# Kernel tuning notes

Hardware: AMD Instinct MI355X
Metric: run time of the kernel (lower is better)

Reference implementation:

```python
import jax, jax.numpy as jnp
import numpy as np

N, E, IN, ED, H, C, G, NC = 50000, 800000, 128, 32, 4, 16, 64, 2
HC = H * C  # 64
NEG_SLOPE = 0.2
EPS = 1e-5


def _layernorm(x, g, b):
    mu = jnp.mean(x, axis=-1, keepdims=True)
    var = jnp.mean((x - mu) ** 2, axis=-1, keepdims=True)
    return (x - mu) * jax.lax.rsqrt(var + EPS) * g + b


def _gat(x, src, dst, edge_attr, W, a_src, a_dst, We, a_edge, b):
    """PyG GATConv (v1) with edge features, concat=True."""
    n = x.shape[0]
    h, c = a_src.shape
    xw = (x @ W).reshape(n, h, c)                       # [N,H,C]
    al_src = jnp.sum(xw * a_src, axis=-1)               # [N,H]
    al_dst = jnp.sum(xw * a_dst, axis=-1)               # [N,H]
    ew = (edge_attr @ We).reshape(-1, h, c)             # [Ef,H,C]
    al_e = jnp.sum(ew * a_edge, axis=-1)                # [Ef,H]
    alpha = al_src[src] + al_dst[dst] + al_e            # [Ef,H]
    alpha = jnp.where(alpha > 0, alpha, NEG_SLOPE * alpha)
    # segment softmax over incoming edges of each dst node
    amax = jax.ops.segment_max(alpha, dst, num_segments=n)
    amax = jnp.where(jnp.isfinite(amax), amax, 0.0)
    ex = jnp.exp(alpha - amax[dst])
    denom = jax.ops.segment_sum(ex, dst, num_segments=n)
    att = ex / (denom[dst] + 1e-16)                     # [Ef,H]
    msg = xw[src] * att[:, :, None]                     # [Ef,H,C]
    out = jax.ops.segment_sum(msg, dst, num_segments=n) # [N,H,C]
    return out.reshape(n, h * c) + b


def setup_inputs() -> dict:
    ks = jax.random.split(jax.random.key(0), 24)
    s = 0.1
    inp = {
        "x": jax.random.normal(ks[0], (N, IN), jnp.float32),
        "edge_attr": jax.random.normal(ks[1], (E, ED), jnp.float32),
        "W1": jax.random.normal(ks[2], (IN, HC), jnp.float32) * s,
        "as1": jax.random.normal(ks[3], (H, C), jnp.float32) * s,
        "ad1": jax.random.normal(ks[4], (H, C), jnp.float32) * s,
        "We1": jax.random.normal(ks[5], (ED, HC), jnp.float32) * s,
        "ae1": jax.random.normal(ks[6], (H, C), jnp.float32) * s,
        "b1": jnp.zeros((HC,), jnp.float32),
        "W2": jax.random.normal(ks[7], (HC, HC), jnp.float32) * s,
        "as2": jax.random.normal(ks[8], (H, C), jnp.float32) * s,
        "ad2": jax.random.normal(ks[9], (H, C), jnp.float32) * s,
        "We2": jax.random.normal(ks[10], (ED, HC), jnp.float32) * s,
        "ae2": jax.random.normal(ks[11], (H, C), jnp.float32) * s,
        "b2": jnp.zeros((HC,), jnp.float32),
        "g1": jnp.ones((HC,), jnp.float32),
        "be1": jnp.zeros((HC,), jnp.float32),
        "fw1": jax.random.normal(ks[12], (HC, 32), jnp.float32) * s,
        "fb1": jnp.zeros((32,), jnp.float32),
        "g2": jnp.ones((32,), jnp.float32),
        "be2": jnp.zeros((32,), jnp.float32),
        "fw2": jax.random.normal(ks[13], (32, NC), jnp.float32) * s,
        "fb2": jnp.zeros((NC,), jnp.float32),
        "edge_index": jax.random.randint(ks[14], (2, E), 0, N, jnp.int64),
        "batch": jnp.sort(jax.random.randint(ks[15], (N,), 0, G, jnp.int64)),
    }
    return inp


def reference(x, edge_attr, W1, as1, ad1, We1, ae1, b1, W2, as2, ad2, We2, ae2,
              b2, g1, be1, fw1, fb1, g2, be2, fw2, fb2, edge_index, batch):
    src, dst = edge_index[0], edge_index[1]
    e = edge_attr.shape[0]
    # add_self_loops with fill_value='mean' (mean of incoming edge_attr per node)
    cnt = jax.ops.segment_sum(jnp.ones((e,), x.dtype), dst, num_segments=N)
    loop_ea = jax.ops.segment_sum(edge_attr, dst, num_segments=N) / jnp.clip(cnt, 1.0)[:, None]
    ar = jnp.arange(N)
    src_f = jnp.concatenate([src, ar])
    dst_f = jnp.concatenate([dst, ar])
    ea_f = jnp.concatenate([edge_attr, loop_ea], axis=0)

    h = _gat(x, src_f, dst_f, ea_f, W1, as1, ad1, We1, ae1, b1)
    h = jax.nn.relu(h)
    h = _layernorm(h, g1, be1)
    h = _gat(h, src_f, dst_f, ea_f, W2, as2, ad2, We2, ae2, b2)
    h = jax.nn.relu(h)
    pooled = jax.ops.segment_max(h, batch, num_segments=G)   # global_max_pool
    pooled = jnp.where(jnp.isfinite(pooled), pooled, 0.0)
    z = pooled @ fw1 + fb1
    z = _layernorm(z, g2, be2)
    z = jax.nn.relu(z)
    # dropout(p=0.4) is identity in eval mode
    z = z @ fw2 + fb2
    return jax.nn.log_softmax(z, axis=1)
```

## Files before the change

kernel.cpp:

```cpp
#include <hip/hip_runtime.h>
#include <math.h>

#define N_NODES 50000
#define N_EDGES 800000
#define IN_DIM 128
#define ED_DIM 32
#define NH 4
#define CH 16
#define HC 64
#define NG 64
#define NCL 2
#define NEG_SLOPE 0.2f
#define LN_EPS 1e-5f
#define NBLK1 196
#define NB_TILE 3125
#define NB_ECH 3125

__global__ void k_scan_local(const int* __restrict__ cnt, int* __restrict__ tmp_ex,
                             int* __restrict__ bsum) {
    __shared__ int sd[256];
    int t = threadIdx.x, idx = blockIdx.x * 256 + t;
    int v = (idx < N_NODES) ? cnt[idx] : 0;
    sd[t] = v; __syncthreads();
    for (int off = 1; off < 256; off <<= 1) {
        int add = (t >= off) ? sd[t - off] : 0;
        __syncthreads();
        sd[t] += add;
        __syncthreads();
    }
    if (idx < N_NODES) tmp_ex[idx] = sd[t] - v;
    if (t == 255) bsum[blockIdx.x] = sd[t];
}

__global__ __launch_bounds__(256) void k_phase1(
        const float* __restrict__ X, const float* __restrict__ W,
        const float* __restrict__ AS, const float* __restrict__ AD,
        float* __restrict__ XW, float* __restrict__ ALS, float* __restrict__ ALD,
        const float* __restrict__ ea,
        const float* __restrict__ We1, const float* __restrict__ ae1,
        const float* __restrict__ We2, const float* __restrict__ ae2,
        float4* __restrict__ ale8,
        const int* __restrict__ dst, int* __restrict__ cnt, int* __restrict__ rank_e) {
    __shared__ float smem[IN_DIM * HC + 16 * IN_DIM];
    int job = blockIdx.x % 3;
    int bid = blockIdx.x / 3;
    int t = threadIdx.x;
    if (job == 0) {
        const int K = IN_DIM;
        float* sW = smem;
        float* sX = smem + K * HC;
        for (int i = t; i < K * HC; i += 256) sW[i] = W[i];
        int nb = bid * 16;
        for (int i = t; i < 16 * K; i += 256) sX[i] = X[(long long)nb * K + i];
        __syncthreads();
        int sub = t >> 6, j = t & 63;
        float acc[4] = {0.f, 0.f, 0.f, 0.f};
        #pragma unroll 8
        for (int k = 0; k < K; ++k) {
            float wv = sW[k * HC + j];
            #pragma unroll
            for (int q = 0; q < 4; ++q) acc[q] += sX[(sub + 4 * q) * K + k] * wv;
        }
        float as_ = AS[j], ad_ = AD[j];
        #pragma unroll
        for (int q = 0; q < 4; ++q) {
            int n = nb + sub + 4 * q;
            XW[(long long)n * HC + j] = acc[q];
            float vs = acc[q] * as_, vd = acc[q] * ad_;
            #pragma unroll
            for (int m = 1; m < 16; m <<= 1) { vs += __shfl_xor(vs, m); vd += __shfl_xor(vd, m); }
            if ((j & 15) == 0) {
                int h = j >> 4;
                ALS[n * 4 + h] = vs; ALD[n * 4 + h] = vd;
            }
        }
    } else if (job == 1) {
        float* sVe = smem;
        float* sE  = smem + 256;
        {
            int d = t >> 3, k = t & 7;
            int l = k >> 2, h = k & 3;
            const float* We = l ? We2 : We1;
            const float* ae = l ? ae2 : ae1;
            float s = 0.f;
            #pragma unroll
            for (int c = 0; c < CH; ++c) s += We[d * HC + h * CH + c] * ae[h * CH + c];
            sVe[d * 8 + k] = s;
        }
        {
            const float4* gsrc = (const float4*)ea + (size_t)bid * 2048;
            #pragma unroll
            for (int r = 0; r < 8; ++r) {
                int i4 = t + r * 256;
                float4 v = gsrc[i4];
                float* dp = sE + (i4 >> 3) * 33 + ((i4 & 7) << 2);
                dp[0] = v.x; dp[1] = v.y; dp[2] = v.z; dp[3] = v.w;
            }
        }
        __syncthreads();
        int e = bid * 256 + t;
        float a[8];
        #pragma unroll
        for (int k = 0; k < 8; ++k) a[k] = 0.f;
        const float* row = sE + t * 33;
        #pragma unroll
        for (int q = 0; q < ED_DIM / 4; ++q) {
            #pragma unroll
            for (int u = 0; u < 4; ++u) {
                float ev = row[q * 4 + u];
                #pragma unroll
                for (int k = 0; k < 8; ++k) a[k] += ev * sVe[(q * 4 + u) * 8 + k];
            }
        }
        float4* out = ale8 + (long long)e * 2;
        out[0] = make_float4(a[0], a[1], a[2], a[3]);
        out[1] = make_float4(a[4], a[5], a[6], a[7]);
    } else {
        int e = bid * 256 + t;
        if (e < N_EDGES) rank_e[e] = atomicAdd(&cnt[dst[e]], 1);
    }
}

__global__ void k_scan_perm(const int* __restrict__ tmp_ex, const int* __restrict__ bsum,
                            int* __restrict__ row_start,
                            const int* __restrict__ dst, const int* __restrict__ srcI,
                            const int* __restrict__ rank_e, int2* __restrict__ perm_src) {
    __shared__ int sd[256];
    __shared__ int sboff[256];
    int t = threadIdx.x;
    int v = (t < NBLK1) ? bsum[t] : 0;
    sd[t] = v; __syncthreads();
    for (int off = 1; off < 256; off <<= 1) {
        int add = (t >= off) ? sd[t - off] : 0;
        __syncthreads();
        sd[t] += add;
        __syncthreads();
    }
    sboff[t] = sd[t] - v;
    __syncthreads();
    if (blockIdx.x < NBLK1) {
        int idx = blockIdx.x * 256 + t;
        if (idx < N_NODES) row_start[idx] = tmp_ex[idx] + sboff[blockIdx.x];
        if (idx == 0) row_start[N_NODES] = N_EDGES;
    } else {
        int e = (blockIdx.x - NBLK1) * 256 + t;
        if (e < N_EDGES) {
            int d = dst[e];
            int pos = tmp_ex[d] + sboff[d >> 8] + rank_e[e];
            perm_src[pos] = make_int2(e, srcI[e]);
        }
    }
}

__global__ __launch_bounds__(256) void k_agg1x(
        const int* __restrict__ rs, const int2* __restrict__ ps,
        const float* __restrict__ ale8,
        const float* __restrict__ ALS, const float* __restrict__ ALD,
        const float* __restrict__ XW, const float* __restrict__ bias,
        const float* __restrict__ gam, const float* __restrict__ bet,
        const float* __restrict__ W2,
        const float* __restrict__ AS2, const float* __restrict__ AD2,
        float* __restrict__ XW2, float* __restrict__ ALS2, float* __restrict__ ALD2) {
    __shared__ float sW2[HC * HC];
    __shared__ float sh[4][HC];
    int t = threadIdx.x;
    for (int i = t; i < HC * HC; i += 256) sW2[i] = W2[i];
    __syncthreads();
    int wid = t >> 6;
    int n = blockIdx.x * 4 + wid;
    int lane = t & 63;
    int h = lane >> 4;
    int e0 = rs[n], e1 = rs[n + 1];
    float adn = ALD[n * 4 + h];
    float acc0 = 0.f, l0 = 0.f, as0 = 0.f;
    float acc1 = 0.f, l1 = 0.f, as1 = 0.f;
    float acc2 = 0.f, l2 = 0.f, as2 = 0.f;
    float acc3 = 0.f, l3 = 0.f, as3 = 0.f;
    int e = e0;
    for (; e + 3 < e1; e += 4) {
        int2 pA = ps[e], pB = ps[e + 1], pC = ps[e + 2], pD = ps[e + 3];
        float aeA = ale8[(long long)pA.x * 8 + h];
        float aeB = ale8[(long long)pB.x * 8 + h];
        float aeC = ale8[(long long)pC.x * 8 + h];
        float aeD = ale8[(long long)pD.x * 8 + h];
        float xA = XW[pA.y * HC + lane];
        float xB = XW[pB.y * HC + lane];
        float xC = XW[pC.y * HC + lane];
        float xD = XW[pD.y * HC + lane];
        float aA = ALS[pA.y * 4 + h] + adn + aeA;
        float aB = ALS[pB.y * 4 + h] + adn + aeB;
        float aC = ALS[pC.y * 4 + h] + adn + aeC;
        float aD = ALS[pD.y * 4 + h] + adn + aeD;
        aA = aA > 0.f ? aA : NEG_SLOPE * aA;
        aB = aB > 0.f ? aB : NEG_SLOPE * aB;
        aC = aC > 0.f ? aC : NEG_SLOPE * aC;
        aD = aD > 0.f ? aD : NEG_SLOPE * aD;
        float qA = __expf(aA), qB = __expf(aB), qC = __expf(aC), qD = __expf(aD);
        acc0 += qA * xA; l0 += qA; as0 += aeA;
        acc1 += qB * xB; l1 += qB; as1 += aeB;
        acc2 += qC * xC; l2 += qC; as2 += aeC;
        acc3 += qD * xD; l3 += qD; as3 += aeD;
    }
    for (; e < e1; ++e) {
        int2 pA = ps[e];
        float aeA = ale8[(long long)pA.x * 8 + h];
        float xA = XW[pA.y * HC + lane];
        float aA = ALS[pA.y * 4 + h] + adn + aeA;
        aA = aA > 0.f ? aA : NEG_SLOPE * aA;
        float qA = __expf(aA);
        acc0 += qA * xA; l0 += qA; as0 += aeA;
    }
    int d = e1 - e0;
    float invd = 1.f / (float)(d > 0 ? d : 1);
    float aSelf = ALS[n * 4 + h] + adn + (as0 + as1 + as2 + as3) * invd;
    aSelf = aSelf > 0.f ? aSelf : NEG_SLOPE * aSelf;
    float pS = __expf(aSelf);
    float acc = (acc0 + acc1) + (acc2 + acc3) + pS * XW[n * HC + lane];
    float l = (l0 + l1) + (l2 + l3) + pS;
    float v = acc / (l + 1e-16f) + bias[lane];
    v = fmaxf(v, 0.f);
    {
        float s1 = v;
        #pragma unroll
        for (int mm = 1; mm < 64; mm <<= 1) s1 += __shfl_xor(s1, mm);
        float mean = s1 * (1.f / 64.f);
        float dd = v - mean;
        float s2 = dd * dd;
        #pragma unroll
        for (int mm = 1; mm < 64; mm <<= 1) s2 += __shfl_xor(s2, mm);
        float var = s2 * (1.f / 64.f);
        v = dd * rsqrtf(var + LN_EPS) * gam[lane] + bet[lane];
    }
    sh[wid][lane] = v;
    float a2 = 0.f;
    #pragma unroll 8
    for (int k = 0; k < HC; ++k) a2 += sh[wid][k] * sW2[k * HC + lane];
    XW2[(long long)n * HC + lane] = a2;
    float vs = a2 * AS2[lane], vd = a2 * AD2[lane];
    #pragma unroll
    for (int m = 1; m < 16; m <<= 1) { vs += __shfl_xor(vs, m); vd += __shfl_xor(vd, m); }
    if ((lane & 15) == 0) {
        ALS2[n * 4 + h] = vs; ALD2[n * 4 + h] = vd;
    }
}

template<bool DO_LN, int LOFF>
__global__ void k_agg(const int* __restrict__ rs, const int2* __restrict__ ps,
                      const float* __restrict__ ale8,
                      const float* __restrict__ ALS, const float* __restrict__ ALD,
                      const float* __restrict__ XW, const float* __restrict__ bias,
                      const float* __restrict__ gam, const float* __restrict__ bet,
                      float* __restrict__ OUT) {
    int n = (blockIdx.x * blockDim.x + threadIdx.x) >> 6;
    if (n >= N_NODES) return;
    int lane = threadIdx.x & 63;
    int h = lane >> 4;
    int e0 = rs[n], e1 = rs[n + 1];
    float adn = ALD[n * 4 + h];
    float acc0 = 0.f, l0 = 0.f, as0 = 0.f;
    float acc1 = 0.f, l1 = 0.f, as1 = 0.f;
    float acc2 = 0.f, l2 = 0.f, as2 = 0.f;
    float acc3 = 0.f, l3 = 0.f, as3 = 0.f;
    int e = e0;
    for (; e + 3 < e1; e += 4) {
        int2 pA = ps[e], pB = ps[e + 1], pC = ps[e + 2], pD = ps[e + 3];
        float aeA = ale8[(long long)pA.x * 8 + LOFF + h];
        float aeB = ale8[(long long)pB.x * 8 + LOFF + h];
        float aeC = ale8[(long long)pC.x * 8 + LOFF + h];
        float aeD = ale8[(long long)pD.x * 8 + LOFF + h];
        float xA = XW[pA.y * HC + lane];
        float xB = XW[pB.y * HC + lane];
        float xC = XW[pC.y * HC + lane];
        float xD = XW[pD.y * HC + lane];
        float aA = ALS[pA.y * 4 + h] + adn + aeA;
        float aB = ALS[pB.y * 4 + h] + adn + aeB;
        float aC = ALS[pC.y * 4 + h] + adn + aeC;
        float aD = ALS[pD.y * 4 + h] + adn + aeD;
        aA = aA > 0.f ? aA : NEG_SLOPE * aA;
        aB = aB > 0.f ? aB : NEG_SLOPE * aB;
        aC = aC > 0.f ? aC : NEG_SLOPE * aC;
        aD = aD > 0.f ? aD : NEG_SLOPE * aD;
        float qA = __expf(aA), qB = __expf(aB), qC = __expf(aC), qD = __expf(aD);
        acc0 += qA * xA; l0 += qA; as0 += aeA;
        acc1 += qB * xB; l1 += qB; as1 += aeB;
        acc2 += qC * xC; l2 += qC; as2 += aeC;
        acc3 += qD * xD; l3 += qD; as3 += aeD;
    }
    for (; e < e1; ++e) {
        int2 pA = ps[e];
        float aeA = ale8[(long long)pA.x * 8 + LOFF + h];
        float xA = XW[pA.y * HC + lane];
        float aA = ALS[pA.y * 4 + h] + adn + aeA;
        aA = aA > 0.f ? aA : NEG_SLOPE * aA;
        float qA = __expf(aA);
        acc0 += qA * xA; l0 += qA; as0 += aeA;
    }
    int d = e1 - e0;
    float invd = 1.f / (float)(d > 0 ? d : 1);
    float aSelf = ALS[n * 4 + h] + adn + (as0 + as1 + as2 + as3) * invd;
    aSelf = aSelf > 0.f ? aSelf : NEG_SLOPE * aSelf;
    float pS = __expf(aSelf);
    float acc = (acc0 + acc1) + (acc2 + acc3) + pS * XW[n * HC + lane];
    float l = (l0 + l1) + (l2 + l3) + pS;
    float v = acc / (l + 1e-16f) + bias[lane];
    v = fmaxf(v, 0.f);
    if (DO_LN) {
        float s1 = v;
        #pragma unroll
        for (int mm = 1; mm < 64; mm <<= 1) s1 += __shfl_xor(s1, mm);
        float mean = s1 * (1.f / 64.f);
        float dd = v - mean;
        float s2 = dd * dd;
        #pragma unroll
        for (int mm = 1; mm < 64; mm <<= 1) s2 += __shfl_xor(s2, mm);
        float var = s2 * (1.f / 64.f);
        v = dd * rsqrtf(var + LN_EPS) * gam[lane] + bet[lane];
    }
    OUT[(long long)n * HC + lane] = v;
}

__global__ void k_pool(const float* __restrict__ H2, const int* __restrict__ batch,
                       float* __restrict__ pooled) {
    int j = threadIdx.x & 63;
    int r = threadIdx.x >> 6;
    int base = blockIdx.x * 128;
    int gcur = -1; float rm = 0.f;
    for (int n = base + r; n < base + 128 && n < N_NODES; n += 4) {
        int g = batch[n];
        if (g != gcur) {
            if (gcur >= 0) atomicMax((unsigned int*)&pooled[gcur * HC + j], __float_as_uint(rm));
            gcur = g; rm = 0.f;
        }
        rm = fmaxf(rm, H2[(long long)n * HC + j]);
    }
    if (gcur >= 0) atomicMax((unsigned int*)&pooled[gcur * HC + j], __float_as_uint(rm));
}

__global__ void k_head(const float* __restrict__ pooled,
                       const float* __restrict__ fw1, const float* __restrict__ fb1,
                       const float* __restrict__ g2, const float* __restrict__ be2,
                       const float* __restrict__ fw2, const float* __restrict__ fb2,
                       float* __restrict__ out) {
    int g = blockIdx.x;
    int j = threadIdx.x;
    float z = 0.f;
    if (j < 32) {
        for (int k = 0; k < HC; ++k) z += pooled[g * HC + k] * fw1[k * 32 + j];
        z += fb1[j];
    }
    float s1 = (j < 32) ? z : 0.f;
    for (int m = 1; m < 32; m <<= 1) s1 += __shfl_xor(s1, m, 32);
    float mean = s1 * (1.f / 32.f);
    float d = z - mean;
    float s2 = (j < 32) ? d * d : 0.f;
    for (int m = 1; m < 32; m <<= 1) s2 += __shfl_xor(s2, m, 32);
    float var = s2 * (1.f / 32.f);
    float zz = 0.f;
    if (j < 32) {
        zz = d * rsqrtf(var + LN_EPS) * g2[j] + be2[j];
        zz = fmaxf(zz, 0.f);
    }
    float p0 = (j < 32) ? zz * fw2[j * NCL + 0] : 0.f;
    float p1 = (j < 32) ? zz * fw2[j * NCL + 1] : 0.f;
    for (int m = 1; m < 32; m <<= 1) { p0 += __shfl_xor(p0, m, 32); p1 += __shfl_xor(p1, m, 32); }
    if (j == 0) {
        float l0 = p0 + fb2[0], l1 = p1 + fb2[1];
        float mx = fmaxf(l0, l1);
        float ls = mx + logf(__expf(l0 - mx) + __expf(l1 - mx));
        out[g * NCL + 0] = l0 - ls;
        out[g * NCL + 1] = l1 - ls;
    }
}

extern "C" void kernel_launch(void* const* d_in, const int* in_sizes, int n_in,
                              void* d_out, int out_size, void* d_ws, size_t ws_size,
                              hipStream_t stream) {
    const float* x   = (const float*)d_in[0];
    const float* ea  = (const float*)d_in[1];
    const float* W1  = (const float*)d_in[2];
    const float* as1 = (const float*)d_in[3];
    const float* ad1 = (const float*)d_in[4];
    const float* We1 = (const float*)d_in[5];
    const float* ae1 = (const float*)d_in[6];
    const float* b1  = (const float*)d_in[7];
    const float* W2  = (const float*)d_in[8];
    const float* as2 = (const float*)d_in[9];
    const float* ad2 = (const float*)d_in[10];
    const float* We2 = (const float*)d_in[11];
    const float* ae2 = (const float*)d_in[12];
    const float* b2  = (const float*)d_in[13];
    const float* g1  = (const float*)d_in[14];
    const float* be1 = (const float*)d_in[15];
    const float* fw1 = (const float*)d_in[16];
    const float* fb1 = (const float*)d_in[17];
    const float* g2  = (const float*)d_in[18];
    const float* be2 = (const float*)d_in[19];
    const float* fw2 = (const float*)d_in[20];
    const float* fb2 = (const float*)d_in[21];
    const int* eidx  = (const int*)d_in[22];
    const int* batch = (const int*)d_in[23];
    const int* srcI = eidx;
    const int* dstI = eidx + N_EDGES;

    char* w = (char*)d_ws;
    auto alloc = [&](size_t bytes) { char* p = w; w += (bytes + 255) & ~(size_t)255; return p; };
    int*   cnt       = (int*)  alloc((size_t)N_NODES * 4);
    int*   row_start = (int*)  alloc((size_t)(N_NODES + 1) * 4);
    int*   rank_e    = (int*)  alloc((size_t)N_EDGES * 4);
    int*   tmp_ex    = (int*)  alloc((size_t)N_NODES * 4);
    int*   bsum      = (int*)  alloc(256 * 4);
    int2*  perm_src  = (int2*) alloc((size_t)N_EDGES * 8);
    float4* ale8     = (float4*)alloc((size_t)N_EDGES * 32);
    float* xw1       = (float*)alloc((size_t)N_NODES * HC * 4);
    float* als1      = (float*)alloc((size_t)N_NODES * 4 * 4);
    float* ald1      = (float*)alloc((size_t)N_NODES * 4 * 4);
    float* xw2       = (float*)alloc((size_t)N_NODES * HC * 4);
    float* als2      = (float*)alloc((size_t)N_NODES * 4 * 4);
    float* ald2      = (float*)alloc((size_t)N_NODES * 4 * 4);
    float* h2        = (float*)alloc((size_t)N_NODES * HC * 4);
    float* pooled    = (float*)alloc((size_t)NG * HC * 4);

    hipMemsetAsync(cnt, 0, (size_t)N_NODES * 4, stream);
    hipMemsetAsync(pooled, 0, (size_t)NG * HC * 4, stream);

    k_phase1<<<3 * NB_TILE, 256, 0, stream>>>(x, W1, as1, ad1, xw1, als1, ald1,
                                              ea, We1, ae1, We2, ae2, ale8,
                                              dstI, cnt, rank_e);
    k_scan_local<<<NBLK1, 256, 0, stream>>>(cnt, tmp_ex, bsum);
    k_scan_perm<<<NBLK1 + NB_ECH, 256, 0, stream>>>(tmp_ex, bsum, row_start,
                                                    dstI, srcI, rank_e, perm_src);

    k_agg1x<<<N_NODES / 4, 256, 0, stream>>>(row_start, perm_src, (const float*)ale8,
                                             als1, ald1, xw1, b1, g1, be1,
                                             W2, as2, ad2, xw2, als2, ald2);
    k_agg<false, 4><<<N_NODES / 4, 256, 0, stream>>>(row_start, perm_src, (const float*)ale8,
                                                     als2, ald2, xw2, b2, nullptr, nullptr, h2);

    k_pool<<<(N_NODES + 127) / 128, 256, 0, stream>>>(h2, batch, pooled);
    k_head<<<NG, 64, 0, stream>>>(pooled, fw1, fb1, g2, be2, fw2, fb2, (float*)d_out);
}
```

Measured before the change: 409.6 us.

## Fuse whole GAT pipeline into one cooperative persistent kernel with grid syncs

```diff
diff --git a/kernel.cpp b/kernel.cpp
--- a/kernel.cpp
+++ b/kernel.cpp
@@ -1,12 +1,13 @@
 #include <hip/hip_runtime.h>
+#include <hip/hip_cooperative_groups.h>
 #include <math.h>
+
+namespace cg = cooperative_groups;
 
 #define N_NODES 50000
 #define N_EDGES 800000
 #define IN_DIM 128
 #define ED_DIM 32
-#define NH 4
-#define CH 16
 #define HC 64
 #define NG 64
 #define NCL 2
@@ -14,22 +15,354 @@
 #define LN_EPS 1e-5f
 #define NBLK1 196
 #define NB_TILE 3125
-#define NB_ECH 3125
-
-__global__ void k_scan_local(const int* __restrict__ cnt, int* __restrict__ tmp_ex,
-                             int* __restrict__ bsum) {
-    __shared__ int sd[256];
-    int t = threadIdx.x, idx = blockIdx.x * 256 + t;
-    int v = (idx < N_NODES) ? cnt[idx] : 0;
-    sd[t] = v; __syncthreads();
-    for (int off = 1; off < 256; off <<= 1) {
-        int add = (t >= off) ? sd[t - off] : 0;
+#define NVB_B 12500
+#define NVB_D 3321
+#define NVB_AGG 12500
+#define NVB_POOL 391
+#define NVB_HEAD 16
+
+struct MParams {
+    const float *x, *ea, *W1, *as1, *ad1, *We1, *ae1, *b1;
+    const float *W2, *as2, *ad2, *We2, *ae2, *b2, *g1, *be1;
+    const float *fw1, *fb1, *g2, *be2, *fw2, *fb2;
+    const int *srcI, *dstI, *batch;
+    int *cnt, *row_start, *rank_e, *tmp_ex, *bsum;
+    int2 *perm_src;
+    float4 *ale8;
+    float *xw1, *als1, *ald1, *xw2, *als2, *ald2, *h2, *pooled, *out;
+};
+
+__global__ __launch_bounds__(256, 8) void mega(MParams p) {
+    cg::grid_group grid = cg::this_grid();
+    __shared__ float smem[4608];
+    int t = threadIdx.x;
+    int nb = gridDim.x;
+
+    for (int i = blockIdx.x * 256 + t; i < N_NODES; i += nb * 256) p.cnt[i] = 0;
+    for (int i = blockIdx.x * 256 + t; i < NG * HC; i += nb * 256) p.pooled[i] = 0.f;
+    grid.sync();
+
+    for (int vb = blockIdx.x; vb < NVB_B; vb += nb) {
+        int job = vb & 3;
+        int bid = vb >> 2;
+        if (job == 0) {
+            float* sX = smem;
+            float* sW = smem + 2048;
+            int nbase = bid * 16;
+            for (int i = t; i < 16 * IN_DIM; i += 256)
+                sX[i] = p.x[(long long)nbase * IN_DIM + i];
+            int sub = t >> 6, j = t & 63;
+            float acc[4] = {0.f, 0.f, 0.f, 0.f};
+            for (int c = 0; c < IN_DIM; c += 32) {
+                if (c) __syncthreads();
+                for (int i = t; i < 32 * HC; i += 256) sW[i] = p.W1[c * HC + i];
+                __syncthreads();
+                #pragma unroll 8
+                for (int kk = 0; kk < 32; ++kk) {
+                    float wv = sW[kk * HC + j];
+                    #pragma unroll
+                    for (int q = 0; q < 4; ++q)
+                        acc[q] += sX[(sub + 4 * q) * IN_DIM + c + kk] * wv;
+                }
+            }
+            float as_ = p.as1[j], ad_ = p.ad1[j];
+            #pragma unroll
+            for (int q = 0; q < 4; ++q) {
+                int n = nbase + sub + 4 * q;
+                p.xw1[(long long)n * HC + j] = acc[q];
+                float vs = acc[q] * as_, vd = acc[q] * ad_;
+                #pragma unroll
+                for (int m = 1; m < 16; m <<= 1) { vs += __shfl_xor(vs, m); vd += __shfl_xor(vd, m); }
+                if ((j & 15) == 0) {
+                    int h = j >> 4;
+                    p.als1[n * 4 + h] = vs; p.ald1[n * 4 + h] = vd;
+                }
+            }
+        } else if (job == 2) {
+            int e = bid * 256 + t;
+            p.rank_e[e] = atomicAdd(&p.cnt[p.dstI[e]], 1);
+        } else {
+            int ebid = (bid << 1) | (job >> 1);
+            float* sVe = smem;
+            float* sE  = smem + 256;
+            {
+                int d = t >> 3, k = t & 7;
+                int l = k >> 2, h = k & 3;
+                const float* We = l ? p.We2 : p.We1;
+                const float* ae = l ? p.ae2 : p.ae1;
+                float s = 0.f;
+                #pragma unroll
+                for (int c = 0; c < 16; ++c) s += We[d * HC + h * 16 + c] * ae[h * 16 + c];
+                sVe[d * 8 + k] = s;
+            }
+            const float4* gsrc = (const float4*)p.ea + (size_t)ebid * 1024;
+            #pragma unroll
+            for (int r = 0; r < 4; ++r) {
+                int i4 = t + r * 256;
+                float4 v = gsrc[i4];
+                float* dp = sE + (i4 >> 3) * 33 + ((i4 & 7) << 2);
+                dp[0] = v.x; dp[1] = v.y; dp[2] = v.z; dp[3] = v.w;
+            }
+            __syncthreads();
+            int el = t & 127;
+            int kb = (t >> 7) * 4;
+            long long e = (long long)ebid * 128 + el;
+            const float* row = sE + el * 33;
+            float a0 = 0.f, a1 = 0.f, a2 = 0.f, a3 = 0.f;
+            #pragma unroll
+            for (int c = 0; c < ED_DIM; ++c) {
+                float ev = row[c];
+                a0 += ev * sVe[c * 8 + kb];
+                a1 += ev * sVe[c * 8 + kb + 1];
+                a2 += ev * sVe[c * 8 + kb + 2];
+                a3 += ev * sVe[c * 8 + kb + 3];
+            }
+            p.ale8[e * 2 + (t >> 7)] = make_float4(a0, a1, a2, a3);
+        }
         __syncthreads();
-        sd[t] += add;
+    }
+    grid.sync();
+
+    {
+        int* sd = (int*)smem;
+        for (int vb = blockIdx.x; vb < NBLK1; vb += nb) {
+            int idx = vb * 256 + t;
+            int v = (idx < N_NODES) ? p.cnt[idx] : 0;
+            sd[t] = v; __syncthreads();
+            for (int off = 1; off < 256; off <<= 1) {
+                int add = (t >= off) ? sd[t - off] : 0;
+                __syncthreads();
+                sd[t] += add;
+                __syncthreads();
+            }
+            if (idx < N_NODES) p.tmp_ex[idx] = sd[t] - v;
+            if (t == 255) p.bsum[vb] = sd[t];
+            __syncthreads();
+        }
+    }
+    grid.sync();
+
+    {
+        int* sd = (int*)smem;
+        int* sboff = sd + 256;
+        for (int vb = blockIdx.x; vb < NVB_D; vb += nb) {
+            int v = (t < NBLK1) ? p.bsum[t] : 0;
+            sd[t] = v; __syncthreads();
+            for (int off = 1; off < 256; off <<= 1) {
+                int add = (t >= off) ? sd[t - off] : 0;
+                __syncthreads();
+                sd[t] += add;
+                __syncthreads();
+            }
+            sboff[t] = sd[t] - v;
+            __syncthreads();
+            if (vb < NBLK1) {
+                int idx = vb * 256 + t;
+                if (idx < N_NODES) p.row_start[idx] = p.tmp_ex[idx] + sboff[vb];
+                if (idx == 0) p.row_start[N_NODES] = N_EDGES;
+            } else {
+                int e = (vb - NBLK1) * 256 + t;
+                int d = p.dstI[e];
+                int pos = p.tmp_ex[d] + sboff[d >> 8] + p.rank_e[e];
+                p.perm_src[pos] = make_int2(e, p.srcI[e]);
+            }
+            __syncthreads();
+        }
+    }
+    grid.sync();
+
+    {
+        float* sW2 = smem;
+        float* sh  = smem + 4096;
+        for (int i = t; i < HC * HC; i += 256) sW2[i] = p.W2[i];
         __syncthreads();
-    }
-    if (idx < N_NODES) tmp_ex[idx] = sd[t] - v;
-    if (t == 255) bsum[blockIdx.x] = sd[t];
+        int wid = t >> 6, lane = t & 63, h = lane >> 4;
+        for (int vb = blockIdx.x; vb < NVB_AGG; vb += nb) {
+            int n = vb * 4 + wid;
+            int e0 = p.row_start[n], e1 = p.row_start[n + 1];
+            float adn = p.ald1[n * 4 + h];
+            float acc0 = 0.f, l0 = 0.f, as0 = 0.f;
+            float acc1 = 0.f, l1 = 0.f, as1 = 0.f;
+            float acc2 = 0.f, l2 = 0.f, as2 = 0.f;
+            float acc3 = 0.f, l3 = 0.f, as3 = 0.f;
+            int e = e0;
+            for (; e + 3 < e1; e += 4) {
+                int2 pA = p.perm_src[e], pB = p.perm_src[e + 1];
+                int2 pC = p.perm_src[e + 2], pD = p.perm_src[e + 3];
+                float aeA = ((const float*)p.ale8)[(long long)pA.x * 8 + h];
+                float aeB = ((const float*)p.ale8)[(long long)pB.x * 8 + h];
+                float aeC = ((const float*)p.ale8)[(long long)pC.x * 8 + h];
+                float aeD = ((const float*)p.ale8)[(long long)pD.x * 8 + h];
+                float xA = p.xw1[pA.y * HC + lane];
+                float xB = p.xw1[pB.y * HC + lane];
+                float xC = p.xw1[pC.y * HC + lane];
+                float xD = p.xw1[pD.y * HC + lane];
+                float aA = p.als1[pA.y * 4 + h] + adn + aeA;
+                float aB = p.als1[pB.y * 4 + h] + adn + aeB;
+                float aC = p.als1[pC.y * 4 + h] + adn + aeC;
+                float aD = p.als1[pD.y * 4 + h] + adn + aeD;
+                aA = aA > 0.f ? aA : NEG_SLOPE * aA;
+                aB = aB > 0.f ? aB : NEG_SLOPE * aB;
+                aC = aC > 0.f ? aC : NEG_SLOPE * aC;
+                aD = aD > 0.f ? aD : NEG_SLOPE * aD;
+                float qA = __expf(aA), qB = __expf(aB), qC = __expf(aC), qD = __expf(aD);
+                acc0 += qA * xA; l0 += qA; as0 += aeA;
+                acc1 += qB * xB; l1 += qB; as1 += aeB;
+                acc2 += qC * xC; l2 += qC; as2 += aeC;
+                acc3 += qD * xD; l3 += qD; as3 += aeD;
+            }
+            for (; e < e1; ++e) {
+                int2 pA = p.perm_src[e];
+                float aeA = ((const float*)p.ale8)[(long long)pA.x * 8 + h];
+                float xA = p.xw1[pA.y * HC + lane];
+                float aA = p.als1[pA.y * 4 + h] + adn + aeA;
+                aA = aA > 0.f ? aA : NEG_SLOPE * aA;
+                float qA = __expf(aA);
+                acc0 += qA * xA; l0 += qA; as0 += aeA;
+            }
+            int d = e1 - e0;
+            float invd = 1.f / (float)(d > 0 ? d : 1);
+            float aSelf = p.als1[n * 4 + h] + adn + (as0 + as1 + as2 + as3) * invd;
+            aSelf = aSelf > 0.f ? aSelf : NEG_SLOPE * aSelf;
+            float pS = __expf(aSelf);
+            float acc = (acc0 + acc1) + (acc2 + acc3) + pS * p.xw1[n * HC + lane];
+            float l = (l0 + l1) + (l2 + l3) + pS;
+            float v = acc / (l + 1e-16f) + p.b1[lane];
+            v = fmaxf(v, 0.f);
+            {
+                float s1 = v;
+                #pragma unroll
+                for (int mm = 1; mm < 64; mm <<= 1) s1 += __shfl_xor(s1, mm);
+                float mean = s1 * (1.f / 64.f);
+                float dd = v - mean;
+                float s2 = dd * dd;
+                #pragma unroll
+                for (int mm = 1; mm < 64; mm <<= 1) s2 += __shfl_xor(s2, mm);
+                float var = s2 * (1.f / 64.f);
+                v = dd * rsqrtf(var + LN_EPS) * p.g1[lane] + p.be1[lane];
+            }
+            sh[wid * HC + lane] = v;
+            float a2 = 0.f;
+            #pragma unroll 8
+            for (int k = 0; k < HC; ++k) a2 += sh[wid * HC + k] * sW2[k * HC + lane];
+            p.xw2[(long long)n * HC + lane] = a2;
+            float vs = a2 * p.as2[lane], vd = a2 * p.ad2[lane];
+            #pragma unroll
+            for (int m = 1; m < 16; m <<= 1) { vs += __shfl_xor(vs, m); vd += __shfl_xor(vd, m); }
+            if ((lane & 15) == 0) {
+                p.als2[n * 4 + h] = vs; p.ald2[n * 4 + h] = vd;
+            }
+        }
+    }
+    grid.sync();
+
+    {
+        int wid = t >> 6, lane = t & 63, h = lane >> 4;
+        for (int vb = blockIdx.x; vb < NVB_AGG; vb += nb) {
+            int n = vb * 4 + wid;
+            int e0 = p.row_start[n], e1 = p.row_start[n + 1];
+            float adn = p.ald2[n * 4 + h];
+            float acc0 = 0.f, l0 = 0.f, as0 = 0.f;
+            float acc1 = 0.f, l1 = 0.f, as1 = 0.f;
+            float acc2 = 0.f, l2 = 0.f, as2 = 0.f;
+            float acc3 = 0.f, l3 = 0.f, as3 = 0.f;
+            int e = e0;
+            for (; e + 3 < e1; e += 4) {
+                int2 pA = p.perm_src[e], pB = p.perm_src[e + 1];
+                int2 pC = p.perm_src[e + 2], pD = p.perm_src[e + 3];
+                float aeA = ((const float*)p.ale8)[(long long)pA.x * 8 + 4 + h];
+                float aeB = ((const float*)p.ale8)[(long long)pB.x * 8 + 4 + h];
+                float aeC = ((const float*)p.ale8)[(long long)pC.x * 8 + 4 + h];
+                float aeD = ((const float*)p.ale8)[(long long)pD.x * 8 + 4 + h];
+                float xA = p.xw2[pA.y * HC + lane];
+                float xB = p.xw2[pB.y * HC + lane];
+                float xC = p.xw2[pC.y * HC + lane];
+                float xD = p.xw2[pD.y * HC + lane];
+                float aA = p.als2[pA.y * 4 + h] + adn + aeA;
+                float aB = p.als2[pB.y * 4 + h] + adn + aeB;
+                float aC = p.als2[pC.y * 4 + h] + adn + aeC;
+                float aD = p.als2[pD.y * 4 + h] + adn + aeD;
+                aA = aA > 0.f ? aA : NEG_SLOPE * aA;
+                aB = aB > 0.f ? aB : NEG_SLOPE * aB;
+                aC = aC > 0.f ? aC : NEG_SLOPE * aC;
+                aD = aD > 0.f ? aD : NEG_SLOPE * aD;
+                float qA = __expf(aA), qB = __expf(aB), qC = __expf(aC), qD = __expf(aD);
+                acc0 += qA * xA; l0 += qA; as0 += aeA;
+                acc1 += qB * xB; l1 += qB; as1 += aeB;
+                acc2 += qC * xC; l2 += qC; as2 += aeC;
+                acc3 += qD * xD; l3 += qD; as3 += aeD;
+            }
+            for (; e < e1; ++e) {
+                int2 pA = p.perm_src[e];
+                float aeA = ((const float*)p.ale8)[(long long)pA.x * 8 + 4 + h];
+                float xA = p.xw2[pA.y * HC + lane];
+                float aA = p.als2[pA.y * 4 + h] + adn + aeA;
+                aA = aA > 0.f ? aA : NEG_SLOPE * aA;
+                float qA = __expf(aA);
+                acc0 += qA * xA; l0 += qA; as0 += aeA;
+            }
+            int d = e1 - e0;
+            float invd = 1.f / (float)(d > 0 ? d : 1);
+            float aSelf = p.als2[n * 4 + h] + adn + (as0 + as1 + as2 + as3) * invd;
+            aSelf = aSelf > 0.f ? aSelf : NEG_SLOPE * aSelf;
+            float pS = __expf(aSelf);
+            float acc = (acc0 + acc1) + (acc2 + acc3) + pS * p.xw2[n * HC + lane];
+            float l = (l0 + l1) + (l2 + l3) + pS;
+            float v = acc / (l + 1e-16f) + p.b2[lane];
+            v = fmaxf(v, 0.f);
+            p.h2[(long long)n * HC + lane] = v;
+        }
+    }
+    grid.sync();
+
+    for (int vb = blockIdx.x; vb < NVB_POOL; vb += nb) {
+        int j = t & 63;
+        int r = t >> 6;
+        int base = vb * 128;
+        int gcur = -1; float rm = 0.f;
+        for (int n = base + r; n < base + 128 && n < N_NODES; n += 4) {
+            int g = p.batch[n];
+            if (g != gcur) {
+                if (gcur >= 0) atomicMax((unsigned int*)&p.pooled[gcur * HC + j], __float_as_uint(rm));
+                gcur = g; rm = 0.f;
+            }
+            rm = fmaxf(rm, p.h2[(long long)n * HC + j]);
+        }
+        if (gcur >= 0) atomicMax((unsigned int*)&p.pooled[gcur * HC + j], __float_as_uint(rm));
+    }
+    grid.sync();
+
+    for (int vb = blockIdx.x; vb < NVB_HEAD; vb += nb) {
+        int g = vb * 4 + (t >> 6);
+        int j = t & 63;
+        float z = 0.f;
+        if (j < 32) {
+            for (int k = 0; k < HC; ++k) z += p.pooled[g * HC + k] * p.fw1[k * 32 + j];
+            z += p.fb1[j];
+        }
+        float s1 = (j < 32) ? z : 0.f;
+        for (int m = 1; m < 32; m <<= 1) s1 += __shfl_xor(s1, m, 32);
+        float mean = s1 * (1.f / 32.f);
+        float d = z - mean;
+        float s2 = (j < 32) ? d * d : 0.f;
+        for (int m = 1; m < 32; m <<= 1) s2 += __shfl_xor(s2, m, 32);
+        float var = s2 * (1.f / 32.f);
+        float zz = 0.f;
+        if (j < 32) {
+            zz = d * rsqrtf(var + LN_EPS) * p.g2[j] + p.be2[j];
+            zz = fmaxf(zz, 0.f);
+        }
+        float p0 = (j < 32) ? zz * p.fw2[j * NCL + 0] : 0.f;
+        float p1 = (j < 32) ? zz * p.fw2[j * NCL + 1] : 0.f;
+        for (int m = 1; m < 32; m <<= 1) { p0 += __shfl_xor(p0, m, 32); p1 += __shfl_xor(p1, m, 32); }
+        if (j == 0) {
+            float l0 = p0 + p.fb2[0], l1 = p1 + p.fb2[1];
+            float mx = fmaxf(l0, l1);
+            float ls = mx + logf(__expf(l0 - mx) + __expf(l1 - mx));
+            p.out[g * NCL + 0] = l0 - ls;
+            p.out[g * NCL + 1] = l1 - ls;
+        }
+    }
 }
 
 __global__ __launch_bounds__(256) void k_phase1(
@@ -69,10 +402,7 @@
             float vs = acc[q] * as_, vd = acc[q] * ad_;
             #pragma unroll
             for (int m = 1; m < 16; m <<= 1) { vs += __shfl_xor(vs, m); vd += __shfl_xor(vd, m); }
-            if ((j & 15) == 0) {
-                int h = j >> 4;
-                ALS[n * 4 + h] = vs; ALD[n * 4 + h] = vd;
-            }
+            if ((j & 15) == 0) { int h = j >> 4; ALS[n * 4 + h] = vs; ALD[n * 4 + h] = vd; }
         }
     } else if (job == 1) {
         float* sVe = smem;
@@ -84,7 +414,7 @@
             const float* ae = l ? ae2 : ae1;
             float s = 0.f;
             #pragma unroll
-            for (int c = 0; c < CH; ++c) s += We[d * HC + h * CH + c] * ae[h * CH + c];
+            for (int c = 0; c < 16; ++c) s += We[d * HC + h * 16 + c] * ae[h * 16 + c];
             sVe[d * 8 + k] = s;
         }
         {
@@ -104,21 +434,34 @@
         for (int k = 0; k < 8; ++k) a[k] = 0.f;
         const float* row = sE + t * 33;
         #pragma unroll
-        for (int q = 0; q < ED_DIM / 4; ++q) {
+        for (int c = 0; c < ED_DIM; ++c) {
+            float ev = row[c];
             #pragma unroll
-            for (int u = 0; u < 4; ++u) {
-                float ev = row[q * 4 + u];
-                #pragma unroll
-                for (int k = 0; k < 8; ++k) a[k] += ev * sVe[(q * 4 + u) * 8 + k];
-            }
-        }
-        float4* out = ale8 + (long long)e * 2;
-        out[0] = make_float4(a[0], a[1], a[2], a[3]);
-        out[1] = make_float4(a[4], a[5], a[6], a[7]);
+            for (int k = 0; k < 8; ++k) a[k] += ev * sVe[c * 8 + k];
+        }
+        float4* outp = ale8 + (long long)e * 2;
+        outp[0] = make_float4(a[0], a[1], a[2], a[3]);
+        outp[1] = make_float4(a[4], a[5], a[6], a[7]);
     } else {
         int e = bid * 256 + t;
         if (e < N_EDGES) rank_e[e] = atomicAdd(&cnt[dst[e]], 1);
     }
+}
+
+__global__ void k_scan_local(const int* __restrict__ cnt, int* __restrict__ tmp_ex,
+                             int* __restrict__ bsum) {
+    __shared__ int sd[256];
+    int t = threadIdx.x, idx = blockIdx.x * 256 + t;
+    int v = (idx < N_NODES) ? cnt[idx] : 0;
+    sd[t] = v; __syncthreads();
+    for (int off = 1; off < 256; off <<= 1) {
+        int add = (t >= off) ? sd[t - off] : 0;
+        __syncthreads();
+        sd[t] += add;
+        __syncthreads();
+    }
+    if (idx < N_NODES) tmp_ex[idx] = sd[t] - v;
+    if (t == 255) bsum[blockIdx.x] = sd[t];
 }
 
 __global__ void k_scan_perm(const int* __restrict__ tmp_ex, const int* __restrict__ bsum,
@@ -239,18 +582,14 @@
     float vs = a2 * AS2[lane], vd = a2 * AD2[lane];
     #pragma unroll
     for (int m = 1; m < 16; m <<= 1) { vs += __shfl_xor(vs, m); vd += __shfl_xor(vd, m); }
-    if ((lane & 15) == 0) {
-        ALS2[n * 4 + h] = vs; ALD2[n * 4 + h] = vd;
-    }
+    if ((lane & 15) == 0) { ALS2[n * 4 + h] = vs; ALD2[n * 4 + h] = vd; }
 }
 
-template<bool DO_LN, int LOFF>
-__global__ void k_agg(const int* __restrict__ rs, const int2* __restrict__ ps,
-                      const float* __restrict__ ale8,
-                      const float* __restrict__ ALS, const float* __restrict__ ALD,
-                      const float* __restrict__ XW, const float* __restrict__ bias,
-                      const float* __restrict__ gam, const float* __restrict__ bet,
-                      float* __restrict__ OUT) {
+__global__ void k_agg2(const int* __restrict__ rs, const int2* __restrict__ ps,
+                       const float* __restrict__ ale8,
+                       const float* __restrict__ ALS, const float* __restrict__ ALD,
+                       const float* __restrict__ XW, const float* __restrict__ bias,
+                       float* __restrict__ OUT) {
     int n = (blockIdx.x * blockDim.x + threadIdx.x) >> 6;
     if (n >= N_NODES) return;
     int lane = threadIdx.x & 63;
@@ -264,10 +603,10 @@
     int e = e0;
     for (; e + 3 < e1; e += 4) {
         int2 pA = ps[e], pB = ps[e + 1], pC = ps[e + 2], pD = ps[e + 3];
-        float aeA = ale8[(long long)pA.x * 8 + LOFF + h];
-        float aeB = ale8[(long long)pB.x * 8 + LOFF + h];
-        float aeC = ale8[(long long)pC.x * 8 + LOFF + h];
-        float aeD = ale8[(long long)pD.x * 8 + LOFF + h];
+        float aeA = ale8[(long long)pA.x * 8 + 4 + h];
+        float aeB = ale8[(long long)pB.x * 8 + 4 + h];
+        float aeC = ale8[(long long)pC.x * 8 + 4 + h];
+        float aeD = ale8[(long long)pD.x * 8 + 4 + h];
         float xA = XW[pA.y * HC + lane];
         float xB = XW[pB.y * HC + lane];
         float xC = XW[pC.y * HC + lane];
@@ -288,7 +627,7 @@
     }
     for (; e < e1; ++e) {
         int2 pA = ps[e];
-        float aeA = ale8[(long long)pA.x * 8 + LOFF + h];
+        float aeA = ale8[(long long)pA.x * 8 + 4 + h];
         float xA = XW[pA.y * HC + lane];
         float aA = ALS[pA.y * 4 + h] + adn + aeA;
         aA = aA > 0.f ? aA : NEG_SLOPE * aA;
@@ -304,18 +643,6 @@
     float l = (l0 + l1) + (l2 + l3) + pS;
     float v = acc / (l + 1e-16f) + bias[lane];
     v = fmaxf(v, 0.f);
-    if (DO_LN) {
-        float s1 = v;
-        #pragma unroll
-        for (int mm = 1; mm < 64; mm <<= 1) s1 += __shfl_xor(s1, mm);
-        float mean = s1 * (1.f / 64.f);
-        float dd = v - mean;
-        float s2 = dd * dd;
-        #pragma unroll
-        for (int mm = 1; mm < 64; mm <<= 1) s2 += __shfl_xor(s2, mm);
-        float var = s2 * (1.f / 64.f);
-        v = dd * rsqrtf(var + LN_EPS) * gam[lane] + bet[lane];
-    }
     OUT[(long long)n * HC + lane] = v;
 }
 
@@ -420,22 +747,58 @@
     float* h2        = (float*)alloc((size_t)N_NODES * HC * 4);
     float* pooled    = (float*)alloc((size_t)NG * HC * 4);
 
+    static int coopBlocks = -1;
+    if (coopBlocks < 0) {
+        int dev = 0; hipGetDevice(&dev);
+        hipDeviceProp_t prop;
+        int nCU = 256, coop = 0;
+        if (hipGetDeviceProperties(&prop, dev) == hipSuccess) {
+            nCU = prop.multiProcessorCount;
+            coop = prop.cooperativeLaunch;
+        }
+        int perCU = 0;
+        if (coop &&
+            hipOccupancyMaxActiveBlocksPerMultiprocessor(&perCU, mega, 256, 0) == hipSuccess &&
+            perCU > 0) {
+            coopBlocks = perCU * nCU;
+        } else {
+            coopBlocks = 0;
+        }
+    }
+
+    if (coopBlocks > 0) {
+        MParams P;
+        P.x = x; P.ea = ea; P.W1 = W1; P.as1 = as1; P.ad1 = ad1;
+        P.We1 = We1; P.ae1 = ae1; P.b1 = b1;
+        P.W2 = W2; P.as2 = as2; P.ad2 = ad2; P.We2 = We2; P.ae2 = ae2; P.b2 = b2;
+        P.g1 = g1; P.be1 = be1; P.fw1 = fw1; P.fb1 = fb1;
+        P.g2 = g2; P.be2 = be2; P.fw2 = fw2; P.fb2 = fb2;
+        P.srcI = srcI; P.dstI = dstI; P.batch = batch;
+        P.cnt = cnt; P.row_start = row_start; P.rank_e = rank_e;
+        P.tmp_ex = tmp_ex; P.bsum = bsum; P.perm_src = perm_src; P.ale8 = ale8;
+        P.xw1 = xw1; P.als1 = als1; P.ald1 = ald1;
+        P.xw2 = xw2; P.als2 = als2; P.ald2 = ald2;
+        P.h2 = h2; P.pooled = pooled; P.out = (float*)d_out;
+        void* kargs[] = { (void*)&P };
+        hipError_t err = hipLaunchCooperativeKernel((void*)mega, dim3(coopBlocks),
+                                                    dim3(256), kargs, 0, stream);
+        if (err == hipSuccess) return;
+        coopBlocks = 0;
+    }
+
     hipMemsetAsync(cnt, 0, (size_t)N_NODES * 4, stream);
     hipMemsetAsync(pooled, 0, (size_t)NG * HC * 4, stream);
-
     k_phase1<<<3 * NB_TILE, 256, 0, stream>>>(x, W1, as1, ad1, xw1, als1, ald1,
                                               ea, We1, ae1, We2, ae2, ale8,
                                               dstI, cnt, rank_e);
     k_scan_local<<<NBLK1, 256, 0, stream>>>(cnt, tmp_ex, bsum);
-    k_scan_perm<<<NBLK1 + NB_ECH, 256, 0, stream>>>(tmp_ex, bsum, row_start,
-                                                    dstI, srcI, rank_e, perm_src);
-
+    k_scan_perm<<<NBLK1 + NB_TILE, 256, 0, stream>>>(tmp_ex, bsum, row_start,
+                                                     dstI, srcI, rank_e, perm_src);
     k_agg1x<<<N_NODES / 4, 256, 0, stream>>>(row_start, perm_src, (const float*)ale8,
                                              als1, ald1, xw1, b1, g1, be1,
                                              W2, as2, ad2, xw2, als2, ald2);
-    k_agg<false, 4><<<N_NODES / 4, 256, 0, stream>>>(row_start, perm_src, (const float*)ale8,
-                                                     als2, ald2, xw2, b2, nullptr, nullptr, h2);
-
+    k_agg2<<<N_NODES / 4, 256, 0, stream>>>(row_start, perm_src, (const float*)ale8,
+                                            als2, ald2, xw2, b2, h2);
     k_pool<<<(N_NODES + 127) / 128, 256, 0, stream>>>(h2, batch, pooled);
     k_head<<<NG, 64, 0, stream>>>(pooled, fw1, fb1, g2, be2, fw2, fb2, (float*)d_out);
 }
```

Measured after the change: 1.539 ms. 276% more time.
